# Performance work log

Measured on AMD Instinct MI355X. Metric: run time of the kernel, lower is better.

The kernel has to match this reference:

```python
import jax, jax.numpy as jnp
import numpy as np
from jax import lax

TOP_K = 8
EPS = 1e-12


def l2_normalize(x, axis):
    sq = jnp.sum(x * x, axis=axis, keepdims=True)
    return x * lax.rsqrt(jnp.maximum(sq, EPS))


def setup_inputs() -> dict:
    key = jax.random.key(0)
    k1, k2, k3, k4 = jax.random.split(key, 4)
    B, N, C = 256, 197, 768
    POOL, LEN = 1024, 8
    x_embed = jax.random.normal(k1, (B, N, C), dtype=jnp.float32)
    prompt = jax.random.uniform(k2, (POOL, LEN, C), dtype=jnp.float32, minval=-1.0, maxval=1.0)
    prompt_key = jax.random.uniform(k3, (POOL, C), dtype=jnp.float32, minval=-1.0, maxval=1.0)
    # kaiming_normal fan_out: std = sqrt(2 / fan_out)
    proj_w = jax.random.normal(k4, (C, C), dtype=jnp.float32) * np.sqrt(2.0 / C).astype(np.float32)
    proj_b = jnp.zeros((C,), dtype=jnp.float32)
    return {"x_embed": x_embed, "prompt": prompt, "prompt_key": prompt_key,
            "proj_w": proj_w, "proj_b": proj_b}


def reference(x_embed, prompt, prompt_key, proj_w, proj_b):
    B = x_embed.shape[0]
    # embedding_key == 'mean'
    x_mean = jnp.mean(x_embed, axis=1)                     # [B, C]
    prompt_norm = l2_normalize(prompt_key, axis=1)         # [P, C]
    x_norm = l2_normalize(x_mean, axis=1)                  # [B, C]
    similarity = x_norm @ prompt_norm.T                    # [B, P]
    _, idx = lax.top_k(similarity, TOP_K)                  # [B, K]
    # gather prompts: [B, K, L, C] -> [B, K*L, C]
    bp = prompt[idx]
    Bk, K, L, C = bp.shape
    batched_prompt = bp.reshape(Bk, K * L, C)
    # projection + residual (dropout in eval mode = identity)
    batched_prompt = batched_prompt @ proj_w.T + proj_b + batched_prompt
    # key loss term
    batched_key_norm = prompt_norm[idx]                    # [B, K, C]
    reduce_sim = jnp.sum(batched_key_norm * x_norm[:, None, :]) / B
    prompted = jnp.concatenate([x_embed[:, :1, :], batched_prompt, x_embed[:, 1:, :]], axis=1)
    return prompted, reduce_sim
```

## Files before the change

kernel.cpp:

```cpp
#include <hip/hip_runtime.h>
#include <float.h>
#include <math.h>

#define B_    256
#define N_    197
#define C_    768
#define POOL_ 1024
#define LEN_  8
#define TOPK_ 8
#define PROWS (POOL_*LEN_)
#define OUTROWS 261

typedef __attribute__((ext_vector_type(8))) short short8_t;
typedef __attribute__((ext_vector_type(4))) float f32x4;

static const size_t OFF_XMEAN = 0;
static const size_t OFF_SIM   = 786432;
static const size_t OFF_ACC   = 1835008;
static const size_t OFF_CNT   = 1835264;
static const size_t OFF_ENT   = 1839360;
static const size_t OFF_ABF   = 2887936;
static const size_t OFF_WBF   = 15470848;

__device__ __forceinline__ unsigned short f2bf(float f) {
    unsigned int u = __float_as_uint(f);
    u += 0x7fffu + ((u >> 16) & 1u);
    return (unsigned short)(u >> 16);
}

__global__ __launch_bounds__(256) void kA(const float* __restrict__ x,
                                          const float* __restrict__ prompt,
                                          const float* __restrict__ projw,
                                          float* __restrict__ xmean,
                                          unsigned short* __restrict__ Abf,
                                          unsigned short* __restrict__ Wbf,
                                          int* __restrict__ cnt,
                                          float* __restrict__ accum) {
    const int bid = blockIdx.x, t = threadIdx.x;
    if (bid < B_ * 3) {
        __shared__ f32x4 red[4][64];
        const int b = bid / 3, seg = bid % 3;
        const int r = t >> 6;
        const int c = t & 63;
        const int c4 = seg * 64 + c;
        const f32x4* xin = (const f32x4*)x + (size_t)b * (N_ * 192) + c4;
        float sx = 0.f, sy = 0.f, sz = 0.f, sw = 0.f;
        #pragma unroll 7
        for (int n = r; n < 196; n += 4) {
            f32x4 v = xin[(size_t)n * 192];
            sx += v.x; sy += v.y; sz += v.z; sw += v.w;
        }
        if (r == 0) {
            f32x4 v = xin[(size_t)196 * 192];
            sx += v.x; sy += v.y; sz += v.z; sw += v.w;
        }
        f32x4 s; s.x = sx; s.y = sy; s.z = sz; s.w = sw;
        red[r][c] = s;
        __syncthreads();
        if (r == 0) {
            f32x4 a = red[0][c], b2 = red[1][c], c2 = red[2][c], d = red[3][c];
            const float inv = 1.0f / (float)N_;
            f32x4 m;
            m.x = (a.x + b2.x + c2.x + d.x) * inv;
            m.y = (a.y + b2.y + c2.y + d.y) * inv;
            m.z = (a.z + b2.z + c2.z + d.z) * inv;
            m.w = (a.w + b2.w + c2.w + d.w) * inv;
            ((f32x4*)xmean)[b * 192 + c4] = m;
        }
    } else if (bid == B_ * 3) {
        ((f32x4*)cnt)[t] = f32x4{0.f, 0.f, 0.f, 0.f};
        if (t == 0) accum[0] = 0.0f;
    } else {
        int i4 = (bid - (B_ * 3 + 1)) * 256 + t;
        float4 v; unsigned short* d;
        if (i4 < (PROWS * C_ / 4)) {
            v = ((const float4*)prompt)[i4];
            d = Abf + (size_t)i4 * 4;
        } else {
            int j4 = i4 - PROWS * C_ / 4;
            v = ((const float4*)projw)[j4];
            d = Wbf + (size_t)j4 * 4;
        }
        ushort4 o; o.x = f2bf(v.x); o.y = f2bf(v.y); o.z = f2bf(v.z); o.w = f2bf(v.w);
        *(ushort4*)d = o;
    }
}

__global__ __launch_bounds__(256) void kS(const float* __restrict__ xmean,
                                          const float* __restrict__ pkey,
                                          float* __restrict__ sim,
                                          const float* __restrict__ x,
                                          float* __restrict__ out) {
    __shared__ float As3[32][36];
    __shared__ float Bs3[32][36];
    __shared__ float sqA[32*8];
    __shared__ float sqB[32*8];
    __shared__ float invs[64];
    const int bid = blockIdx.x, t = threadIdx.x;

    if (bid < 256) {
        const int m0 = (bid >> 5) * 32, n0 = (bid & 31) * 32;
        const int lrow = t >> 3, lc = (t & 7) * 4;
        const int ty = t >> 4, tx = t & 15;
        float a00 = 0.f, a01 = 0.f, a10 = 0.f, a11 = 0.f;
        float sqa = 0.f, sqb = 0.f;
        float4 va = *(const float4*)&xmean[(size_t)(m0 + lrow) * C_ + lc];
        float4 vb = *(const float4*)&pkey [(size_t)(n0 + lrow) * C_ + lc];
        for (int k0 = 0; k0 < C_; k0 += 32) {
            __syncthreads();
            *(float4*)&As3[lrow][lc] = va;
            *(float4*)&Bs3[lrow][lc] = vb;
            sqa += va.x*va.x + va.y*va.y + va.z*va.z + va.w*va.w;
            sqb += vb.x*vb.x + vb.y*vb.y + vb.z*vb.z + vb.w*vb.w;
            __syncthreads();
            if (k0 + 32 < C_) {
                va = *(const float4*)&xmean[(size_t)(m0 + lrow) * C_ + k0 + 32 + lc];
                vb = *(const float4*)&pkey [(size_t)(n0 + lrow) * C_ + k0 + 32 + lc];
            }
            #pragma unroll
            for (int kk = 0; kk < 32; kk += 4) {
                float4 A0 = *(const float4*)&As3[ty*2][kk];
                float4 A1 = *(const float4*)&As3[ty*2+1][kk];
                float4 B0 = *(const float4*)&Bs3[tx*2][kk];
                float4 B1 = *(const float4*)&Bs3[tx*2+1][kk];
                a00 += A0.x*B0.x; a00 += A0.y*B0.y; a00 += A0.z*B0.z; a00 += A0.w*B0.w;
                a01 += A0.x*B1.x; a01 += A0.y*B1.y; a01 += A0.z*B1.z; a01 += A0.w*B1.w;
                a10 += A1.x*B0.x; a10 += A1.y*B0.y; a10 += A1.z*B0.z; a10 += A1.w*B0.w;
                a11 += A1.x*B1.x; a11 += A1.y*B1.y; a11 += A1.z*B1.z; a11 += A1.w*B1.w;
            }
        }
        sqA[lrow*8 + (t & 7)] = sqa;
        sqB[lrow*8 + (t & 7)] = sqb;
        __syncthreads();
        if (t < 64) {
            const float* s = (t < 32) ? sqA : sqB;
            const int rr = t & 31;
            float tot = 0.f;
            #pragma unroll
            for (int j = 0; j < 8; ++j) tot += s[rr*8 + j];
            invs[t] = 1.0f / sqrtf(fmaxf(tot, 1e-12f));
        }
        __syncthreads();
        const float im0 = invs[ty*2], im1 = invs[ty*2 + 1];
        const float ip0 = invs[32 + tx*2], ip1 = invs[32 + tx*2 + 1];
        sim[(size_t)(m0 + ty*2    ) * POOL_ + n0 + tx*2    ] = a00 * im0 * ip0;
        sim[(size_t)(m0 + ty*2    ) * POOL_ + n0 + tx*2 + 1] = a01 * im0 * ip1;
        sim[(size_t)(m0 + ty*2 + 1) * POOL_ + n0 + tx*2    ] = a10 * im1 * ip0;
        sim[(size_t)(m0 + ty*2 + 1) * POOL_ + n0 + tx*2 + 1] = a11 * im1 * ip1;
    } else {
        const int cb = bid - 256;
        const int b = cb / 3, seg = cb % 3;
        const int r = t >> 6, c = t & 63;
        const int c4 = seg * 64 + c;
        const f32x4* xin  = (const f32x4*)x   + (size_t)b * (N_ * 192) + c4;
        f32x4*       outb = (f32x4*)out       + (size_t)b * (OUTROWS * 192) + c4;
        #pragma unroll 7
        for (int n = r; n < 196; n += 4) {
            f32x4 v = xin[(size_t)n * 192];
            int orow = (n == 0) ? 0 : (64 + n);
            __builtin_nontemporal_store(v, &outb[(size_t)orow * 192]);
        }
        if (r == 0) {
            f32x4 v = xin[(size_t)196 * 192];
            __builtin_nontemporal_store(v, &outb[(size_t)260 * 192]);
        }
    }
}

__global__ __launch_bounds__(256) void kT(const float* __restrict__ sim,
                                          int* __restrict__ cnt,
                                          int* __restrict__ entries,
                                          float* __restrict__ accum) {
    __shared__ float vals[POOL_];
    __shared__ float wv[4];
    __shared__ int   wi[4];
    __shared__ int   sidx[TOPK_];
    const int b = blockIdx.x, t = threadIdx.x;
    const int wave = t >> 6;
    #pragma unroll
    for (int i = 0; i < 4; ++i) vals[t + 256*i] = sim[(size_t)b * POOL_ + t + 256*i];
    __syncthreads();
    float sumv = 0.0f;
    for (int k = 0; k < TOPK_; ++k) {
        float bv = -FLT_MAX; int bi = POOL_;
        #pragma unroll
        for (int i = 0; i < 4; ++i) {
            int n = t + 256*i;
            float v = vals[n];
            if (v > bv) { bv = v; bi = n; }
        }
        #pragma unroll
        for (int off = 32; off > 0; off >>= 1) {
            float v2 = __shfl_down(bv, off);
            int   i2 = __shfl_down(bi, off);
            if (v2 > bv || (v2 == bv && i2 < bi)) { bv = v2; bi = i2; }
        }
        if ((t & 63) == 0) { wv[wave] = bv; wi[wave] = bi; }
        __syncthreads();
        if (t == 0) {
            float fv = wv[0]; int fi = wi[0];
            #pragma unroll
            for (int w = 1; w < 4; ++w) {
                float v2 = wv[w]; int i2 = wi[w];
                if (v2 > fv || (v2 == fv && i2 < fi)) { fv = v2; fi = i2; }
            }
            sidx[k] = fi;
            sumv += fv;
            vals[fi] = -FLT_MAX;
        }
        __syncthreads();
    }
    if (t < TOPK_) {
        const int p = sidx[t];
        const int pos = atomicAdd(&cnt[p], 1);
        entries[(p << 8) + pos] = (b << 3) | t;
    }
    if (t == 0) atomicAdd(accum, sumv);
}

__global__ __launch_bounds__(256) void kG(const unsigned short* __restrict__ A,
                                          const unsigned short* __restrict__ W,
                                          const float* __restrict__ bias,
                                          const float* __restrict__ resid,
                                          const int* __restrict__ cnt,
                                          const int* __restrict__ entries,
                                          const float* __restrict__ accum,
                                          float* __restrict__ out) {
    __shared__ short As5[2][64*32];
    __shared__ short Bs5[2][128*32];
    const int tid = threadIdx.x;
    const int bid = blockIdx.x;
    if (bid == 0 && tid == 0)
        out[(size_t)B_ * OUTROWS * C_] = accum[0] * (1.0f / (float)B_);

    const int m0 = (bid / 6) * 64, n0 = (bid % 6) * 128;
    const int wave = tid >> 6, lane = tid & 63;
    const int quad = lane >> 4, lr = lane & 15;
    const int srow = tid >> 2;
    const int scol = (tid & 3) * 8;

    f32x4 acc[4][2] = {};

    auto stage = [&](int buf, int kt) {
        const int k0 = kt * 32;
        __builtin_amdgcn_global_load_lds(
            (const __attribute__((address_space(1))) void*)&A[(size_t)(m0 + srow) * C_ + k0 + scol],
            (__attribute__((address_space(3))) void*)&As5[buf][srow*32 + scol], 16, 0, 0);
        __builtin_amdgcn_global_load_lds(
            (const __attribute__((address_space(1))) void*)&W[(size_t)(n0 + srow) * C_ + k0 + scol],
            (__attribute__((address_space(3))) void*)&Bs5[buf][srow*32 + scol], 16, 0, 0);
        __builtin_amdgcn_global_load_lds(
            (const __attribute__((address_space(1))) void*)&W[(size_t)(n0 + 64 + srow) * C_ + k0 + scol],
            (__attribute__((address_space(3))) void*)&Bs5[buf][(64 + srow)*32 + scol], 16, 0, 0);
    };
    auto compute = [&](int buf) {
        short8_t af[4], bf[2];
        #pragma unroll
        for (int i = 0; i < 4; ++i)
            af[i] = *(const short8_t*)&As5[buf][(i*16 + lr)*32 + quad*8];
        #pragma unroll
        for (int j = 0; j < 2; ++j)
            bf[j] = *(const short8_t*)&Bs5[buf][(wave*32 + j*16 + lr)*32 + quad*8];
        #pragma unroll
        for (int i = 0; i < 4; ++i)
            #pragma unroll
            for (int j = 0; j < 2; ++j)
                acc[i][j] = __builtin_amdgcn_mfma_f32_16x16x32_bf16(af[i], bf[j], acc[i][j], 0, 0, 0);
    };

    stage(0, 0);
    __syncthreads();
    int cur = 0;
    for (int kt = 0; kt < 23; ++kt) {
        stage(cur ^ 1, kt + 1);
        compute(cur);
        __syncthreads();
        cur ^= 1;
    }
    compute(cur);

    const float bn0 = bias[n0 + wave*32 + lr];
    const float bn1 = bias[n0 + wave*32 + 16 + lr];
    const int ncol = n0 + wave*32 + lr;
    #pragma unroll
    for (int i = 0; i < 4; ++i) {
        const int m  = m0 + i*16 + quad*4;
        const int p  = m >> 3;
        const int lb = m & 7;
        const int c  = cnt[p];
        if (c != 0) {
            float vals[2][4];
            #pragma unroll
            for (int r = 0; r < 4; ++r) {
                vals[0][r] = acc[i][0][r] + bn0 + resid[(size_t)(m + r) * C_ + ncol];
                vals[1][r] = acc[i][1][r] + bn1 + resid[(size_t)(m + r) * C_ + ncol + 16];
            }
            for (int h = 0; h < c; ++h) {
                const int bk = entries[(p << 8) + h];
                const size_t obase =
                    (size_t)((bk >> 3) * OUTROWS + 1 + (bk & 7) * 8 + lb) * C_ + ncol;
                #pragma unroll
                for (int r = 0; r < 4; ++r) {
                    out[obase + (size_t)r * C_]      = vals[0][r];
                    out[obase + (size_t)r * C_ + 16] = vals[1][r];
                }
            }
        }
    }
}

extern "C" void kernel_launch(void* const* d_in, const int* in_sizes, int n_in,
                              void* d_out, int out_size, void* d_ws, size_t ws_size,
                              hipStream_t stream) {
    const float* x_embed = (const float*)d_in[0];
    const float* prompt  = (const float*)d_in[1];
    const float* pkey    = (const float*)d_in[2];
    const float* projw   = (const float*)d_in[3];
    const float* projb   = (const float*)d_in[4];
    float* out = (float*)d_out;
    char* ws = (char*)d_ws;

    float*          xmean   = (float*)(ws + OFF_XMEAN);
    float*          sim     = (float*)(ws + OFF_SIM);
    float*          acc     = (float*)(ws + OFF_ACC);
    int*            cnt     = (int*)(ws + OFF_CNT);
    int*            ent     = (int*)(ws + OFF_ENT);
    unsigned short* Abf     = (unsigned short*)(ws + OFF_ABF);
    unsigned short* Wbf     = (unsigned short*)(ws + OFF_WBF);

    const int convBlocks = (PROWS * C_ / 4 + 768 * 768 / 4) / 256;
    kA<<<B_ * 3 + 1 + convBlocks, 256, 0, stream>>>(x_embed, prompt, projw,
                                                    xmean, Abf, Wbf, cnt, acc);
    kS<<<1024, 256, 0, stream>>>(xmean, pkey, sim, x_embed, out);
    kT<<<B_, 256, 0, stream>>>(sim, cnt, ent, acc);
    kG<<<768, 256, 0, stream>>>(Abf, Wbf, projb, prompt, cnt, ent, acc, out);
}
```

Baseline: 411.0 us.

## Fuse x_embed copy into mean kernel and skip GEMM tiles with unselected prompts

The passthrough copy of x_embed into the output moves into the mean-reduction kernel, so x_embed is read once instead of twice, and the similarity kernel loses its copy blocks. The projection GEMM now exits early for 64-row tiles whose 8 prompts were never selected by any batch top-k, skipping work for unused pool entries. This adds a dependency on the count array being correct, and leaves the mean kernel doing more store traffic per block.

```diff
diff --git a/kernel.cpp b/kernel.cpp
--- a/kernel.cpp
+++ b/kernel.cpp
@@ -31,6 +31,7 @@
 __global__ __launch_bounds__(256) void kA(const float* __restrict__ x,
                                           const float* __restrict__ prompt,
                                           const float* __restrict__ projw,
+                                          float* __restrict__ out,
                                           float* __restrict__ xmean,
                                           unsigned short* __restrict__ Abf,
                                           unsigned short* __restrict__ Wbf,
@@ -43,16 +44,20 @@
         const int r = t >> 6;
         const int c = t & 63;
         const int c4 = seg * 64 + c;
-        const f32x4* xin = (const f32x4*)x + (size_t)b * (N_ * 192) + c4;
+        const f32x4* xin  = (const f32x4*)x   + (size_t)b * (N_ * 192) + c4;
+        f32x4*       outb = (f32x4*)out       + (size_t)b * (OUTROWS * 192) + c4;
         float sx = 0.f, sy = 0.f, sz = 0.f, sw = 0.f;
         #pragma unroll 7
         for (int n = r; n < 196; n += 4) {
-            f32x4 v = xin[(size_t)n * 192];
+            f32x4 v = __builtin_nontemporal_load(&xin[(size_t)n * 192]);
             sx += v.x; sy += v.y; sz += v.z; sw += v.w;
+            int orow = (n == 0) ? 0 : (64 + n);
+            __builtin_nontemporal_store(v, &outb[(size_t)orow * 192]);
         }
         if (r == 0) {
-            f32x4 v = xin[(size_t)196 * 192];
+            f32x4 v = __builtin_nontemporal_load(&xin[(size_t)196 * 192]);
             sx += v.x; sy += v.y; sz += v.z; sw += v.w;
+            __builtin_nontemporal_store(v, &outb[(size_t)260 * 192]);
         }
         f32x4 s; s.x = sx; s.y = sy; s.z = sz; s.w = sw;
         red[r][c] = s;
@@ -88,83 +93,61 @@
 
 __global__ __launch_bounds__(256) void kS(const float* __restrict__ xmean,
                                           const float* __restrict__ pkey,
-                                          float* __restrict__ sim,
-                                          const float* __restrict__ x,
-                                          float* __restrict__ out) {
+                                          float* __restrict__ sim) {
     __shared__ float As3[32][36];
     __shared__ float Bs3[32][36];
     __shared__ float sqA[32*8];
     __shared__ float sqB[32*8];
     __shared__ float invs[64];
     const int bid = blockIdx.x, t = threadIdx.x;
-
-    if (bid < 256) {
-        const int m0 = (bid >> 5) * 32, n0 = (bid & 31) * 32;
-        const int lrow = t >> 3, lc = (t & 7) * 4;
-        const int ty = t >> 4, tx = t & 15;
-        float a00 = 0.f, a01 = 0.f, a10 = 0.f, a11 = 0.f;
-        float sqa = 0.f, sqb = 0.f;
-        float4 va = *(const float4*)&xmean[(size_t)(m0 + lrow) * C_ + lc];
-        float4 vb = *(const float4*)&pkey [(size_t)(n0 + lrow) * C_ + lc];
-        for (int k0 = 0; k0 < C_; k0 += 32) {
-            __syncthreads();
-            *(float4*)&As3[lrow][lc] = va;
-            *(float4*)&Bs3[lrow][lc] = vb;
-            sqa += va.x*va.x + va.y*va.y + va.z*va.z + va.w*va.w;
-            sqb += vb.x*vb.x + vb.y*vb.y + vb.z*vb.z + vb.w*vb.w;
-            __syncthreads();
-            if (k0 + 32 < C_) {
-                va = *(const float4*)&xmean[(size_t)(m0 + lrow) * C_ + k0 + 32 + lc];
-                vb = *(const float4*)&pkey [(size_t)(n0 + lrow) * C_ + k0 + 32 + lc];
-            }
-            #pragma unroll
-            for (int kk = 0; kk < 32; kk += 4) {
-                float4 A0 = *(const float4*)&As3[ty*2][kk];
-                float4 A1 = *(const float4*)&As3[ty*2+1][kk];
-                float4 B0 = *(const float4*)&Bs3[tx*2][kk];
-                float4 B1 = *(const float4*)&Bs3[tx*2+1][kk];
-                a00 += A0.x*B0.x; a00 += A0.y*B0.y; a00 += A0.z*B0.z; a00 += A0.w*B0.w;
-                a01 += A0.x*B1.x; a01 += A0.y*B1.y; a01 += A0.z*B1.z; a01 += A0.w*B1.w;
-                a10 += A1.x*B0.x; a10 += A1.y*B0.y; a10 += A1.z*B0.z; a10 += A1.w*B0.w;
-                a11 += A1.x*B1.x; a11 += A1.y*B1.y; a11 += A1.z*B1.z; a11 += A1.w*B1.w;
-            }
-        }
-        sqA[lrow*8 + (t & 7)] = sqa;
-        sqB[lrow*8 + (t & 7)] = sqb;
-        __syncthreads();
-        if (t < 64) {
-            const float* s = (t < 32) ? sqA : sqB;
-            const int rr = t & 31;
-            float tot = 0.f;
-            #pragma unroll
-            for (int j = 0; j < 8; ++j) tot += s[rr*8 + j];
-            invs[t] = 1.0f / sqrtf(fmaxf(tot, 1e-12f));
-        }
-        __syncthreads();
-        const float im0 = invs[ty*2], im1 = invs[ty*2 + 1];
-        const float ip0 = invs[32 + tx*2], ip1 = invs[32 + tx*2 + 1];
-        sim[(size_t)(m0 + ty*2    ) * POOL_ + n0 + tx*2    ] = a00 * im0 * ip0;
-        sim[(size_t)(m0 + ty*2    ) * POOL_ + n0 + tx*2 + 1] = a01 * im0 * ip1;
-        sim[(size_t)(m0 + ty*2 + 1) * POOL_ + n0 + tx*2    ] = a10 * im1 * ip0;
-        sim[(size_t)(m0 + ty*2 + 1) * POOL_ + n0 + tx*2 + 1] = a11 * im1 * ip1;
-    } else {
-        const int cb = bid - 256;
-        const int b = cb / 3, seg = cb % 3;
-        const int r = t >> 6, c = t & 63;
-        const int c4 = seg * 64 + c;
-        const f32x4* xin  = (const f32x4*)x   + (size_t)b * (N_ * 192) + c4;
-        f32x4*       outb = (f32x4*)out       + (size_t)b * (OUTROWS * 192) + c4;
-        #pragma unroll 7
-        for (int n = r; n < 196; n += 4) {
-            f32x4 v = xin[(size_t)n * 192];
-            int orow = (n == 0) ? 0 : (64 + n);
-            __builtin_nontemporal_store(v, &outb[(size_t)orow * 192]);
-        }
-        if (r == 0) {
-            f32x4 v = xin[(size_t)196 * 192];
-            __builtin_nontemporal_store(v, &outb[(size_t)260 * 192]);
-        }
-    }
+    const int m0 = (bid >> 5) * 32, n0 = (bid & 31) * 32;
+    const int lrow = t >> 3, lc = (t & 7) * 4;
+    const int ty = t >> 4, tx = t & 15;
+    float a00 = 0.f, a01 = 0.f, a10 = 0.f, a11 = 0.f;
+    float sqa = 0.f, sqb = 0.f;
+    float4 va = *(const float4*)&xmean[(size_t)(m0 + lrow) * C_ + lc];
+    float4 vb = *(const float4*)&pkey [(size_t)(n0 + lrow) * C_ + lc];
+    for (int k0 = 0; k0 < C_; k0 += 32) {
+        __syncthreads();
+        *(float4*)&As3[lrow][lc] = va;
+        *(float4*)&Bs3[lrow][lc] = vb;
+        sqa += va.x*va.x + va.y*va.y + va.z*va.z + va.w*va.w;
+        sqb += vb.x*vb.x + vb.y*vb.y + vb.z*vb.z + vb.w*vb.w;
+        __syncthreads();
+        if (k0 + 32 < C_) {
+            va = *(const float4*)&xmean[(size_t)(m0 + lrow) * C_ + k0 + 32 + lc];
+            vb = *(const float4*)&pkey [(size_t)(n0 + lrow) * C_ + k0 + 32 + lc];
+        }
+        #pragma unroll
+        for (int kk = 0; kk < 32; kk += 4) {
+            float4 A0 = *(const float4*)&As3[ty*2][kk];
+            float4 A1 = *(const float4*)&As3[ty*2+1][kk];
+            float4 B0 = *(const float4*)&Bs3[tx*2][kk];
+            float4 B1 = *(const float4*)&Bs3[tx*2+1][kk];
+            a00 += A0.x*B0.x; a00 += A0.y*B0.y; a00 += A0.z*B0.z; a00 += A0.w*B0.w;
+            a01 += A0.x*B1.x; a01 += A0.y*B1.y; a01 += A0.z*B1.z; a01 += A0.w*B1.w;
+            a10 += A1.x*B0.x; a10 += A1.y*B0.y; a10 += A1.z*B0.z; a10 += A1.w*B0.w;
+            a11 += A1.x*B1.x; a11 += A1.y*B1.y; a11 += A1.z*B1.z; a11 += A1.w*B1.w;
+        }
+    }
+    sqA[lrow*8 + (t & 7)] = sqa;
+    sqB[lrow*8 + (t & 7)] = sqb;
+    __syncthreads();
+    if (t < 64) {
+        const float* s = (t < 32) ? sqA : sqB;
+        const int rr = t & 31;
+        float tot = 0.f;
+        #pragma unroll
+        for (int j = 0; j < 8; ++j) tot += s[rr*8 + j];
+        invs[t] = 1.0f / sqrtf(fmaxf(tot, 1e-12f));
+    }
+    __syncthreads();
+    const float im0 = invs[ty*2], im1 = invs[ty*2 + 1];
+    const float ip0 = invs[32 + tx*2], ip1 = invs[32 + tx*2 + 1];
+    sim[(size_t)(m0 + ty*2    ) * POOL_ + n0 + tx*2    ] = a00 * im0 * ip0;
+    sim[(size_t)(m0 + ty*2    ) * POOL_ + n0 + tx*2 + 1] = a01 * im0 * ip1;
+    sim[(size_t)(m0 + ty*2 + 1) * POOL_ + n0 + tx*2    ] = a10 * im1 * ip0;
+    sim[(size_t)(m0 + ty*2 + 1) * POOL_ + n0 + tx*2 + 1] = a11 * im1 * ip1;
 }
 
 __global__ __launch_bounds__(256) void kT(const float* __restrict__ sim,
@@ -234,6 +217,13 @@
         out[(size_t)B_ * OUTROWS * C_] = accum[0] * (1.0f / (float)B_);
 
     const int m0 = (bid / 6) * 64, n0 = (bid % 6) * 128;
+
+    const int pbase = m0 >> 3;
+    int anyhit = 0;
+    #pragma unroll
+    for (int e = 0; e < 8; ++e) anyhit |= cnt[pbase + e];
+    if (anyhit == 0) return;
+
     const int wave = tid >> 6, lane = tid & 63;
     const int quad = lane >> 4, lr = lane & 15;
     const int srow = tid >> 2;
@@ -330,8 +320,8 @@
 
     const int convBlocks = (PROWS * C_ / 4 + 768 * 768 / 4) / 256;
     kA<<<B_ * 3 + 1 + convBlocks, 256, 0, stream>>>(x_embed, prompt, projw,
-                                                    xmean, Abf, Wbf, cnt, acc);
-    kS<<<1024, 256, 0, stream>>>(xmean, pkey, sim, x_embed, out);
+                                                    out, xmean, Abf, Wbf, cnt, acc);
+    kS<<<256, 256, 0, stream>>>(xmean, pkey, sim);
     kT<<<B_, 256, 0, stream>>>(sim, cnt, ent, acc);
     kG<<<768, 256, 0, stream>>>(Abf, Wbf, projb, prompt, cnt, ent, acc, out);
 }
```

After: 399.3 us. 2.8% less time.
